# Kernel optimization log

Measured on AMD Instinct MI355X. Metric: run time of the kernel, lower is better.

The kernel has to match this reference:

```python
import jax, jax.numpy as jnp
import numpy as np

DIM = 128
NUM_LAYERS = 4
VOCAB = 32000
B, S = 32, 256


def setup_inputs() -> dict:
    key = jax.random.key(0)
    ks = jax.random.split(key, 8)
    sc = 1.0 / np.sqrt(DIM)
    return {
        "x": jax.random.randint(ks[0], (B, S), 0, VOCAB, dtype=jnp.int32),
        "emb": jax.random.normal(ks[1], (VOCAB, DIM), jnp.float32) * 0.02,
        "W_ih": jax.random.uniform(ks[2], (NUM_LAYERS, 4 * DIM, DIM), jnp.float32, -sc, sc),
        "W_hh": jax.random.uniform(ks[3], (NUM_LAYERS, 4 * DIM, DIM), jnp.float32, -sc, sc),
        "b_ih": jax.random.uniform(ks[4], (NUM_LAYERS, 4 * DIM), jnp.float32, -sc, sc),
        "b_hh": jax.random.uniform(ks[5], (NUM_LAYERS, 4 * DIM), jnp.float32, -sc, sc),
        "ln_gamma": jnp.ones((DIM,), jnp.float32),
        "ln_beta": jnp.zeros((DIM,), jnp.float32),
        "head_W": jax.random.uniform(ks[6], (VOCAB, DIM), jnp.float32, -sc, sc),
        "head_b": jnp.zeros((VOCAB,), jnp.float32),
    }


def _lstm_layer(h_seq, Wih, Whh, bih, bhh):
    # h_seq: [B,S,D]. Precompute input contributions for all timesteps.
    xW = jnp.einsum("bsd,gd->bsg", h_seq, Wih) + bih + bhh  # [B,S,4D]
    xW = jnp.swapaxes(xW, 0, 1)  # [S,B,4D] for scan over time
    bsz = h_seq.shape[0]
    h0 = jnp.zeros((bsz, DIM), h_seq.dtype)
    c0 = jnp.zeros((bsz, DIM), h_seq.dtype)

    def step(carry, xw_t):
        h, c = carry
        gates = xw_t + h @ Whh.T  # [B,4D]
        i, f, g, o = jnp.split(gates, 4, axis=-1)  # torch gate order i,f,g,o
        i = jax.nn.sigmoid(i)
        f = jax.nn.sigmoid(f)
        g = jnp.tanh(g)
        o = jax.nn.sigmoid(o)
        c = f * c + i * g
        h = o * jnp.tanh(c)
        return (h, c), h

    _, hs = jax.lax.scan(step, (h0, c0), xW)
    return jnp.swapaxes(hs, 0, 1)  # [B,S,D]


def reference(x, emb, W_ih, W_hh, b_ih, b_hh, ln_gamma, ln_beta, head_W, head_b):
    h = emb[x]  # [B,S,D]
    for l in range(NUM_LAYERS):
        h = _lstm_layer(h, W_ih[l], W_hh[l], b_ih[l], b_hh[l])
    # LayerNorm over last dim (eps=1e-5, torch default)
    mu = jnp.mean(h, axis=-1, keepdims=True)
    var = jnp.mean(jnp.square(h - mu), axis=-1, keepdims=True)
    hn = (h - mu) * jax.lax.rsqrt(var + 1e-5) * ln_gamma + ln_beta
    return jnp.einsum("bsd,vd->bsv", hn, head_W) + head_b  # [B,S,V]
```

## Files before the change

kernel.cpp:

```cpp
#include <hip/hip_runtime.h>
#include <hip/hip_bf16.h>

#define DIM 128
#define G4 512
#define NL 4
#define VOCAB 32000
#define BB 32
#define SS 256
#define ROWS (BB*SS)

typedef __attribute__((ext_vector_type(8))) short short8;
typedef __attribute__((ext_vector_type(4))) float f32x4;
typedef __attribute__((ext_vector_type(4))) unsigned int uint4v;
typedef __attribute__((ext_vector_type(2))) _Float16 h2;

__device__ __forceinline__ float fexp_(float x){ return __builtin_amdgcn_exp2f(x * 1.44269504088896f); }
__device__ __forceinline__ float frcp_(float x){ return __builtin_amdgcn_rcpf(x); }
__device__ __forceinline__ float sigm_(float x){ return frcp_(1.f + fexp_(-x)); }
__device__ __forceinline__ float tanh_(float x){
    float ax = fabsf(x);
    float e = fexp_(-2.f * ax);
    float t = (1.f - e) * frcp_(1.f + e);
    return x < 0.f ? -t : t;
}
__device__ __forceinline__ h2 mkh(float a, float b){ h2 r; r.x = (_Float16)a; r.y = (_Float16)b; return r; }

#if __has_builtin(__builtin_amdgcn_fdot2)
#define FDOT2(w, d, acc) acc = __builtin_amdgcn_fdot2(w, d, acc, false);
#else
#define FDOT2(w, d, acc) acc = fmaf((float)(w).x, (float)(d).x, fmaf((float)(w).y, (float)(d).y, acc));
#endif
#define B2H(u) __builtin_bit_cast(h2, (unsigned)(u))
#define F2US(x) ((unsigned long long)__builtin_bit_cast(unsigned short, (_Float16)(x)))

#define WD32(p) h2 p##0,p##1,p##2,p##3,p##4,p##5,p##6,p##7,p##8,p##9,p##10,p##11, \
                   p##12,p##13,p##14,p##15,p##16,p##17,p##18,p##19,p##20,p##21,p##22,p##23, \
                   p##24,p##25,p##26,p##27,p##28,p##29,p##30,p##31;
#define WCVT32(p, src) { float4 t_; \
    t_=(src)[0];  p##0 =mkh(t_.x,t_.y); p##1 =mkh(t_.z,t_.w); \
    t_=(src)[1];  p##2 =mkh(t_.x,t_.y); p##3 =mkh(t_.z,t_.w); \
    t_=(src)[2];  p##4 =mkh(t_.x,t_.y); p##5 =mkh(t_.z,t_.w); \
    t_=(src)[3];  p##6 =mkh(t_.x,t_.y); p##7 =mkh(t_.z,t_.w); \
    t_=(src)[4];  p##8 =mkh(t_.x,t_.y); p##9 =mkh(t_.z,t_.w); \
    t_=(src)[5];  p##10=mkh(t_.x,t_.y); p##11=mkh(t_.z,t_.w); \
    t_=(src)[6];  p##12=mkh(t_.x,t_.y); p##13=mkh(t_.z,t_.w); \
    t_=(src)[7];  p##14=mkh(t_.x,t_.y); p##15=mkh(t_.z,t_.w); \
    t_=(src)[8];  p##16=mkh(t_.x,t_.y); p##17=mkh(t_.z,t_.w); \
    t_=(src)[9];  p##18=mkh(t_.x,t_.y); p##19=mkh(t_.z,t_.w); \
    t_=(src)[10]; p##20=mkh(t_.x,t_.y); p##21=mkh(t_.z,t_.w); \
    t_=(src)[11]; p##22=mkh(t_.x,t_.y); p##23=mkh(t_.z,t_.w); \
    t_=(src)[12]; p##24=mkh(t_.x,t_.y); p##25=mkh(t_.z,t_.w); \
    t_=(src)[13]; p##26=mkh(t_.x,t_.y); p##27=mkh(t_.z,t_.w); \
    t_=(src)[14]; p##28=mkh(t_.x,t_.y); p##29=mkh(t_.z,t_.w); \
    t_=(src)[15]; p##30=mkh(t_.x,t_.y); p##31=mkh(t_.z,t_.w); }
#define DT32(p, acc) \
    FDOT2(p##0,d0,acc)  FDOT2(p##1,d1,acc)  FDOT2(p##2,d2,acc)  FDOT2(p##3,d3,acc) \
    FDOT2(p##4,d4,acc)  FDOT2(p##5,d5,acc)  FDOT2(p##6,d6,acc)  FDOT2(p##7,d7,acc) \
    FDOT2(p##8,d8,acc)  FDOT2(p##9,d9,acc)  FDOT2(p##10,d10,acc) FDOT2(p##11,d11,acc) \
    FDOT2(p##12,d12,acc) FDOT2(p##13,d13,acc) FDOT2(p##14,d14,acc) FDOT2(p##15,d15,acc) \
    FDOT2(p##16,d16,acc) FDOT2(p##17,d17,acc) FDOT2(p##18,d18,acc) FDOT2(p##19,d19,acc) \
    FDOT2(p##20,d20,acc) FDOT2(p##21,d21,acc) FDOT2(p##22,d22,acc) FDOT2(p##23,d23,acc) \
    FDOT2(p##24,d24,acc) FDOT2(p##25,d25,acc) FDOT2(p##26,d26,acc) FDOT2(p##27,d27,acc) \
    FDOT2(p##28,d28,acc) FDOT2(p##29,d29,acc) FDOT2(p##30,d30,acc) FDOT2(p##31,d31,acc)
#define RD32(base) { const uint4v* hc_ = (const uint4v*)(base); \
    uint4v q0_=hc_[0], q1_=hc_[1], q2_=hc_[2], q3_=hc_[3], \
           q4_=hc_[4], q5_=hc_[5], q6_=hc_[6], q7_=hc_[7]; \
    d0=B2H(q0_.x); d1=B2H(q0_.y); d2=B2H(q0_.z); d3=B2H(q0_.w); \
    d4=B2H(q1_.x); d5=B2H(q1_.y); d6=B2H(q1_.z); d7=B2H(q1_.w); \
    d8=B2H(q2_.x); d9=B2H(q2_.y); d10=B2H(q2_.z); d11=B2H(q2_.w); \
    d12=B2H(q3_.x); d13=B2H(q3_.y); d14=B2H(q3_.z); d15=B2H(q3_.w); \
    d16=B2H(q4_.x); d17=B2H(q4_.y); d18=B2H(q4_.z); d19=B2H(q4_.w); \
    d20=B2H(q5_.x); d21=B2H(q5_.y); d22=B2H(q5_.z); d23=B2H(q5_.w); \
    d24=B2H(q6_.x); d25=B2H(q6_.y); d26=B2H(q6_.z); d27=B2H(q6_.w); \
    d28=B2H(q7_.x); d29=B2H(q7_.y); d30=B2H(q7_.z); d31=B2H(q7_.w); }

#define W_DECL_ALL \
    float4 w0,w1,w2,w3,w4,w5,w6,w7,w8,w9,w10,w11,w12,w13,w14,w15, \
           w16,w17,w18,w19,w20,w21,w22,w23,w24,w25,w26,w27,w28,w29,w30,w31;
#define W_LOAD(i) w##i = wr[i];
#define W_LOAD_ALL \
    W_LOAD(0) W_LOAD(1) W_LOAD(2) W_LOAD(3) W_LOAD(4) W_LOAD(5) W_LOAD(6) W_LOAD(7) \
    W_LOAD(8) W_LOAD(9) W_LOAD(10) W_LOAD(11) W_LOAD(12) W_LOAD(13) W_LOAD(14) W_LOAD(15) \
    W_LOAD(16) W_LOAD(17) W_LOAD(18) W_LOAD(19) W_LOAD(20) W_LOAD(21) W_LOAD(22) W_LOAD(23) \
    W_LOAD(24) W_LOAD(25) W_LOAD(26) W_LOAD(27) W_LOAD(28) W_LOAD(29) W_LOAD(30) W_LOAD(31)
#define FMA1(i, acc) acc = fmaf(h4[i].x, w##i.x, fmaf(h4[i].y, w##i.y, \
                      fmaf(h4[i].z, w##i.z, fmaf(h4[i].w, w##i.w, acc))));
#define DOT128(a0,a1,a2,a3) \
    FMA1(0,a0) FMA1(1,a0) FMA1(2,a0) FMA1(3,a0) FMA1(4,a0) FMA1(5,a0) FMA1(6,a0) FMA1(7,a0) \
    FMA1(8,a1) FMA1(9,a1) FMA1(10,a1) FMA1(11,a1) FMA1(12,a1) FMA1(13,a1) FMA1(14,a1) FMA1(15,a1) \
    FMA1(16,a2) FMA1(17,a2) FMA1(18,a2) FMA1(19,a2) FMA1(20,a2) FMA1(21,a2) FMA1(22,a2) FMA1(23,a2) \
    FMA1(24,a3) FMA1(25,a3) FMA1(26,a3) FMA1(27,a3) FMA1(28,a3) FMA1(29,a3) FMA1(30,a3) FMA1(31,a3)

__global__ void k_zero(int* __restrict__ f){ if (threadIdx.x < 96) f[threadIdx.x] = 0; }

__global__ void k_embed(const int* __restrict__ x, const float* __restrict__ emb,
                        float* __restrict__ hseq){
    int i = blockIdx.x * blockDim.x + threadIdx.x;
    int row = i >> 5;
    int d4  = i & 31;
    int tok = x[row];
    ((float4*)hseq)[i] = ((const float4*)emb)[tok * 32 + d4];
}

__global__ __launch_bounds__(512, 2) void k_xw(const float* __restrict__ hseq,
                                               const float* Wih,
                                               const float* __restrict__ bih,
                                               const float* __restrict__ bhh,
                                               float* xw){
    __shared__ float hs[32 * DIM];
    int g = threadIdx.x;
    int r0 = blockIdx.x * 32;
    {
        const float4* src = (const float4*)(hseq + (size_t)r0 * DIM);
        float4* dst = (float4*)hs;
        for (int j = g; j < 32 * 32; j += 512) dst[j] = src[j];
    }
    int gg = ((g & 3) << 7) + (g >> 2);
    const float4* wr = (const float4*)(Wih + (size_t)gg * DIM);
    W_DECL_ALL
    W_LOAD_ALL
    float bias = bih[gg] + bhh[gg];
    __syncthreads();
    for (int r = 0; r < 32; ++r){
        const float4* h4 = (const float4*)(hs + r * DIM);
        float a0 = bias, a1 = 0.f, a2 = 0.f, a3 = 0.f;
        DOT128(a0, a1, a2, a3)
        xw[(size_t)(r0 + r) * G4 + g] = (a0 + a1) + (a2 + a3);
    }
}

#define SCAN_STEP(XC, CH, I) { \
        h2 d0,d1,d2,d3,d4,d5,d6,d7,d8,d9,d10,d11,d12,d13,d14,d15, \
           d16,d17,d18,d19,d20,d21,d22,d23,d24,d25,d26,d27,d28,d29,d30,d31; \
        float s0 = XC.x, s1 = XC.y; \
        RD32(&hb[p][0]) \
        DT32(pA, s0) DT32(pC, s1) \
        RD32(&hb[p][64]) \
        DT32(pB, s0) DT32(pD, s1) \
        float o0 = __shfl_xor(s0, 1), o1 = __shfl_xor(s1, 1); \
        float i_pre = w ? o0 : s0, f_pre = w ? o1 : s1; \
        float g_pre = w ? s0 : o0, o_pre = w ? s1 : o1; \
        float iv = sigm_(i_pre), fv = sigm_(f_pre); \
        float gv = tanh_(g_pre), ov = sigm_(o_pre); \
        cc = fv * cc + iv * gv; \
        float h = ov * tanh_(cc); \
        if (!w) hb[p ^ 1][ci] = (_Float16)h; \
        else    stg[(CH) & 1][I][ci] = h; \
        __syncthreads(); \
        p ^= 1; }

#define XN_DOT(I) { \
        h2 d0,d1,d2,d3,d4,d5,d6,d7,d8,d9,d10,d11,d12,d13,d14,d15, \
           d16,d17,d18,d19,d20,d21,d22,d23,d24,d25,d26,d27,d28,d29,d30,d31; \
        float nx = biasv.x, ny = biasv.y; \
        RD32(hpF + (I) * 128) \
        DT32(pE, nx) DT32(pG, ny) \
        RD32(hpF + (I) * 128 + 64) \
        DT32(pF, nx) DT32(pH, ny) \
        xn##I.x = nx; xn##I.y = ny; }

__global__ __launch_bounds__(256, 1) void k_fused(
    const float* __restrict__ xw0,
    const float* Wih, const float* Whh,
    const float* __restrict__ bih, const float* __restrict__ bhh,
    unsigned long long* hf16,
    float* hseq3,
    int* flags)
{
    __shared__ _Float16 hb[2][DIM];
    __shared__ float    stg[2][16][DIM];
    __shared__ __align__(16) unsigned long long hp[512];
    const int tid = threadIdx.x;
    const int l = blockIdx.x >> 5, b = blockIdx.x & 31;
    const int ci = tid >> 1, w = tid & 1;
    const _Float16* hpF = (const _Float16*)hp;

    WD32(pA) WD32(pB) WD32(pC) WD32(pD)
    {
        const float* Wl = Whh + (size_t)l * G4 * DIM;
        const float4* r0 = (const float4*)(Wl + (size_t)((2 * w    ) * DIM + ci) * DIM);
        const float4* r1 = (const float4*)(Wl + (size_t)((2 * w + 1) * DIM + ci) * DIM);
        WCVT32(pA, r0) WCVT32(pB, r0 + 16)
        WCVT32(pC, r1) WCVT32(pD, r1 + 16)
    }
    WD32(pE) WD32(pF) WD32(pG) WD32(pH)
    float2 biasv = {0.f, 0.f};
    if (l > 0){
        const float* Vl = Wih + (size_t)l * G4 * DIM;
        const float4* q0 = (const float4*)(Vl + (size_t)((2 * w    ) * DIM + ci) * DIM);
        const float4* q1 = (const float4*)(Vl + (size_t)((2 * w + 1) * DIM + ci) * DIM);
        WCVT32(pE, q0) WCVT32(pF, q0 + 16)
        WCVT32(pG, q1) WCVT32(pH, q1 + 16)
        biasv.x = bih[l * G4 + (2 * w    ) * DIM + ci] + bhh[l * G4 + (2 * w    ) * DIM + ci];
        biasv.y = bih[l * G4 + (2 * w + 1) * DIM + ci] + bhh[l * G4 + (2 * w + 1) * DIM + ci];
    }
    unsigned long long*       pub = hf16 + (size_t)(l * 32 + b) * 8192;
    const unsigned long long* src = hf16 + (size_t)((l - 1) * 32 + b) * 8192;
    int* myflag = flags + (l * 32 + b);
    const int* inflag = flags + ((l - 1) * 32 + b);
    const float2* xw2 = (const float2*)(xw0 + (size_t)b * SS * G4);
    float* hout = hseq3 + (size_t)b * SS * DIM;

    float cc = 0.f;
    if (tid < DIM) hb[0][tid] = (_Float16)0.f;
    __syncthreads();
    int p = 0;
    int seen = 0;
    float2 xq0,xq1,xq2,xq3,xq4,xq5,xq6,xq7,xq8,xq9,xq10,xq11,xq12,xq13,xq14,xq15;
    float2 xn0,xn1,xn2,xn3,xn4,xn5,xn6,xn7,xn8,xn9,xn10,xn11,xn12,xn13,xn14,xn15;

#define BLOCK_WAIT(TGT) { int t_ = (TGT); if (seen < t_){ \
        if (tid == 0){ while (__hip_atomic_load(inflag, __ATOMIC_ACQUIRE, \
            __HIP_MEMORY_SCOPE_AGENT) < t_) __builtin_amdgcn_s_sleep(4); } \
        __syncthreads(); seen = t_; } }
#define STAGE(C) { const unsigned long long* s_ = src + (size_t)(C) * 512; \
        hp[tid]       = __hip_atomic_load(s_ + tid,       __ATOMIC_RELAXED, __HIP_MEMORY_SCOPE_AGENT); \
        hp[tid + 256] = __hip_atomic_load(s_ + tid + 256, __ATOMIC_RELAXED, __HIP_MEMORY_SCOPE_AGENT); }
#define FLUSH_PUB(C) { \
    _Pragma("unroll") \
    for (int j = 0; j < 2; ++j){ \
        int idx = j * 256 + tid; \
        int r = idx >> 5, c4 = idx & 31; \
        float4 v = *(const float4*)&stg[(C) & 1][r][c4 * 4]; \
        unsigned long long bits = F2US(v.x) | (F2US(v.y) << 16) | (F2US(v.z) << 32) | (F2US(v.w) << 48); \
        __hip_atomic_store(pub + (size_t)((C) * 16 + r) * 32 + c4, bits, \
                           __ATOMIC_RELAXED, __HIP_MEMORY_SCOPE_AGENT); \
    } }
#define FLUSH_F32(C) { \
    _Pragma("unroll") \
    for (int j = 0; j < 2; ++j){ \
        int idx = j * 256 + tid; \
        int r = idx >> 5, c4 = idx & 31; \
        float4 v = *(const float4*)&stg[(C) & 1][r][c4 * 4]; \
        *(float4*)(hout + (size_t)((C) * 16 + r) * DIM + c4 * 4) = v; \
    } }
#define XQ_FROM_XN \
    xq0=xn0; xq1=xn1; xq2=xn2; xq3=xn3; xq4=xn4; xq5=xn5; xq6=xn6; xq7=xn7; \
    xq8=xn8; xq9=xn9; xq10=xn10; xq11=xn11; xq12=xn12; xq13=xn13; xq14=xn14; xq15=xn15;

    if (l > 0){
        BLOCK_WAIT(1)
        STAGE(0)
        __syncthreads();
        XN_DOT(0)  XN_DOT(1)  XN_DOT(2)  XN_DOT(3)  XN_DOT(4)  XN_DOT(5)  XN_DOT(6)  XN_DOT(7)
        XN_DOT(8)  XN_DOT(9)  XN_DOT(10) XN_DOT(11) XN_DOT(12) XN_DOT(13) XN_DOT(14) XN_DOT(15)
        XQ_FROM_XN
    }

#pragma unroll 1
    for (int c = 0; c < 16; ++c){
        if (c > 0){
            if (l < 3) FLUSH_PUB(c - 1)
            else       FLUSH_F32(c - 1)
        }
        if (l == 0){
            const int t0 = c * 16;
            xq0  = xw2[(t0 +  0) * 256 + tid]; xq1  = xw2[(t0 +  1) * 256 + tid];
            xq2  = xw2[(t0 +  2) * 256 + tid]; xq3  = xw2[(t0 +  3) * 256 + tid];
            xq4  = xw2[(t0 +  4) * 256 + tid]; xq5  = xw2[(t0 +  5) * 256 + tid];
            xq6  = xw2[(t0 +  6) * 256 + tid]; xq7  = xw2[(t0 +  7) * 256 + tid];
            xq8  = xw2[(t0 +  8) * 256 + tid]; xq9  = xw2[(t0 +  9) * 256 + tid];
            xq10 = xw2[(t0 + 10) * 256 + tid]; xq11 = xw2[(t0 + 11) * 256 + tid];
            xq12 = xw2[(t0 + 12) * 256 + tid]; xq13 = xw2[(t0 + 13) * 256 + tid];
            xq14 = xw2[(t0 + 14) * 256 + tid]; xq15 = xw2[(t0 + 15) * 256 + tid];
        } else if (c < 15){
            BLOCK_WAIT(c + 2)
            STAGE(c + 1)
        }
        __syncthreads();
        if (l < 3 && c > 0 && tid == 0)
            __hip_atomic_store(myflag, c, __ATOMIC_RELEASE, __HIP_MEMORY_SCOPE_AGENT);
        const bool doXN = (l > 0) && (c < 15);
        if (doXN) XN_DOT(0)   SCAN_STEP(xq0,  c, 0)
        if (doXN) XN_DOT(1)   SCAN_STEP(xq1,  c, 1)
        if (doXN) XN_DOT(2)   SCAN_STEP(xq2,  c, 2)
        if (doXN) XN_DOT(3)   SCAN_STEP(xq3,  c, 3)
        if (doXN) XN_DOT(4)   SCAN_STEP(xq4,  c, 4)
        if (doXN) XN_DOT(5)   SCAN_STEP(xq5,  c, 5)
        if (doXN) XN_DOT(6)   SCAN_STEP(xq6,  c, 6)
        if (doXN) XN_DOT(7)   SCAN_STEP(xq7,  c, 7)
        if (doXN) XN_DOT(8)   SCAN_STEP(xq8,  c, 8)
        if (doXN) XN_DOT(9)   SCAN_STEP(xq9,  c, 9)
        if (doXN) XN_DOT(10)  SCAN_STEP(xq10, c, 10)
        if (doXN) XN_DOT(11)  SCAN_STEP(xq11, c, 11)
        if (doXN) XN_DOT(12)  SCAN_STEP(xq12, c, 12)
        if (doXN) XN_DOT(13)  SCAN_STEP(xq13, c, 13)
        if (doXN) XN_DOT(14)  SCAN_STEP(xq14, c, 14)
        if (doXN) XN_DOT(15)  SCAN_STEP(xq15, c, 15)
        if (doXN){ XQ_FROM_XN }
    }
    if (l < 3){
        FLUSH_PUB(15)
        __syncthreads();
        if (tid == 0)
            __hip_atomic_store(myflag, 16, __ATOMIC_RELEASE, __HIP_MEMORY_SCOPE_AGENT);
    } else {
        FLUSH_F32(15)
    }
#undef BLOCK_WAIT
#undef STAGE
#undef FLUSH_PUB
#undef FLUSH_F32
#undef XQ_FROM_XN
}

__global__ void k_ln(const float* __restrict__ hseq, const float* __restrict__ gamma,
                     const float* __restrict__ beta, __hip_bfloat16* __restrict__ hn){
    int wid = threadIdx.x >> 6;
    int lane = threadIdx.x & 63;
    int row = blockIdx.x * 4 + wid;
    float2 hv = ((const float2*)(hseq + (size_t)row * DIM))[lane];
    float s = hv.x + hv.y;
    float sq = fmaf(hv.x, hv.x, hv.y * hv.y);
    for (int off = 32; off; off >>= 1){ s += __shfl_xor(s, off); sq += __shfl_xor(sq, off); }
    float mu = s * (1.f / 128.f);
    float var = sq * (1.f / 128.f) - mu * mu;
    float inv = rsqrtf(var + 1e-5f);
    float2 gv = ((const float2*)gamma)[lane];
    float2 bv = ((const float2*)beta)[lane];
    __hip_bfloat162 pr;
    pr.x = __float2bfloat16((hv.x - mu) * inv * gv.x + bv.x);
    pr.y = __float2bfloat16((hv.y - mu) * inv * gv.y + bv.y);
    ((__hip_bfloat162*)hn)[(size_t)row * 64 + lane] = pr;
}

__global__ void k_cvt(const float* __restrict__ w, __hip_bfloat16* __restrict__ wb){
    int i = blockIdx.x * blockDim.x + threadIdx.x;
    float4 v = ((const float4*)w)[i];
    __hip_bfloat162 p0, p1;
    p0.x = __float2bfloat16(v.x); p0.y = __float2bfloat16(v.y);
    p1.x = __float2bfloat16(v.z); p1.y = __float2bfloat16(v.w);
    ((__hip_bfloat162*)wb)[2 * i]     = p0;
    ((__hip_bfloat162*)wb)[2 * i + 1] = p1;
}

__global__ __launch_bounds__(256) void k_head(const __hip_bfloat16* __restrict__ hn,
                                              const __hip_bfloat16* __restrict__ wb,
                                              const float* __restrict__ head_b,
                                              float* __restrict__ out){
    int bn = blockIdx.x;
    int bm = blockIdx.y;
    int wid = threadIdx.x >> 6;
    int lane = threadIdx.x & 63;
    int wr = wid >> 1, wc = wid & 1;
    int row0 = bm * 128 + wr * 64;
    int col0 = bn * 128 + wc * 64;
    const short* A  = (const short*)hn;
    const short* Bp = (const short*)wb;
    f32x4 zero = {0.f, 0.f, 0.f, 0.f};
    f32x4 acc[4][4];
#pragma unroll
    for (int i = 0; i < 4; ++i)
#pragma unroll
        for (int j = 0; j < 4; ++j) acc[i][j] = zero;
    int lrow = lane & 15;
    int kgr = (lane >> 4) * 8;
#pragma unroll
    for (int ks = 0; ks < 4; ++ks){
        short8 a[4], bf[4];
#pragma unroll
        for (int mi = 0; mi < 4; ++mi)
            a[mi] = *(const short8*)(A + (size_t)(row0 + mi * 16 + lrow) * DIM + ks * 32 + kgr);
#pragma unroll
        for (int ni = 0; ni < 4; ++ni)
            bf[ni] = *(const short8*)(Bp + (size_t)(col0 + ni * 16 + lrow) * DIM + ks * 32 + kgr);
#pragma unroll
        for (int mi = 0; mi < 4; ++mi)
#pragma unroll
            for (int ni = 0; ni < 4; ++ni)
                acc[mi][ni] = __builtin_amdgcn_mfma_f32_16x16x32_bf16(bf[ni], a[mi], acc[mi][ni], 0, 0, 0);
    }
    int csub = (lane >> 4) * 4;
#pragma unroll
    for (int ni = 0; ni < 4; ++ni){
        int cbase = col0 + ni * 16 + csub;
        float4 b4 = ((const float4*)head_b)[cbase >> 2];
#pragma unroll
        for (int mi = 0; mi < 4; ++mi){
            int row = row0 + mi * 16 + lrow;
            f32x4 v;
            v[0] = acc[mi][ni][0] + b4.x;
            v[1] = acc[mi][ni][1] + b4.y;
            v[2] = acc[mi][ni][2] + b4.z;
            v[3] = acc[mi][ni][3] + b4.w;
            __builtin_nontemporal_store(v, (f32x4*)(out + (size_t)row * VOCAB + cbase));
        }
    }
}

extern "C" void kernel_launch(void* const* d_in, const int* in_sizes, int n_in,
                              void* d_out, int out_size, void* d_ws, size_t ws_size,
                              hipStream_t stream){
    const int*   x     = (const int*)  d_in[0];
    const float* emb   = (const float*)d_in[1];
    const float* Wih   = (const float*)d_in[2];
    const float* Whh   = (const float*)d_in[3];
    const float* bih   = (const float*)d_in[4];
    const float* bhh   = (const float*)d_in[5];
    const float* gamma = (const float*)d_in[6];
    const float* beta  = (const float*)d_in[7];
    const float* headW = (const float*)d_in[8];
    const float* headb = (const float*)d_in[9];
    float* out = (float*)d_out;

    char* ws = (char*)d_ws;
    float* xw0  = (float*)ws;
    float* hseq = (float*)(ws + (16u << 20));
    __hip_bfloat16* hn = (__hip_bfloat16*)(ws + (20u << 20));
    __hip_bfloat16* wb = (__hip_bfloat16*)(ws + (22u << 20));

    char* ob = (char*)d_out;
    unsigned long long* hf16 = (unsigned long long*)ob;
    int* flags = (int*)(ob + (6u << 20));

    k_embed<<<1024, 256, 0, stream>>>(x, emb, hseq);
    k_cvt  <<<4000, 256, 0, stream>>>(headW, wb);
    k_xw   <<<256, 512, 0, stream>>>(hseq, Wih, bih, bhh, xw0);
    k_zero <<<1, 128, 0, stream>>>(flags);
    k_fused<<<128, 256, 0, stream>>>(xw0, Wih, Whh, bih, bhh, hf16, hseq, flags);
    k_ln   <<<2048, 256, 0, stream>>>(hseq, gamma, beta, hn);
    k_head <<<dim3(250, 64), 256, 0, stream>>>(hn, wb, headb, out);
}
```

Before: 782.8 us.

## Fuse embedding into xw, LayerNorm into LSTM kernel, halve chunk size

Folds the embedding gather into the input-projection kernel and stores the layer-0 gate pre-activations as fp16 instead of fp32. LayerNorm moves into the last layer's flush inside the fused LSTM kernel, so the separate embed and LN kernels and the fp32 hidden-sequence round trip go away. Pipeline chunks shrink from 16 to 8 timesteps, which shortens the wait between layers in the wavefront at the cost of more flag syncs. It also pads LDS with a large unused array, presumably to limit co-residency, and adds a min-blocks hint on the head GEMM. The fp16 pre-activations cost some precision.

```diff
diff --git a/kernel.cpp b/kernel.cpp
--- a/kernel.cpp
+++ b/kernel.cpp
@@ -24,6 +24,15 @@
     return x < 0.f ? -t : t;
 }
 __device__ __forceinline__ h2 mkh(float a, float b){ h2 r; r.x = (_Float16)a; r.y = (_Float16)b; return r; }
+__device__ __forceinline__ unsigned long long f2bf_(float f){
+    unsigned u = __float_as_uint(f);
+    u += 0x7fffu + ((u >> 16) & 1u);
+    return (unsigned long long)(u >> 16);
+}
+__device__ __forceinline__ float2 c2f(unsigned u){
+    h2 v = __builtin_bit_cast(h2, u);
+    float2 r; r.x = (float)v.x; r.y = (float)v.y; return r;
+}
 
 #if __has_builtin(__builtin_amdgcn_fdot2)
 #define FDOT2(w, d, acc) acc = __builtin_amdgcn_fdot2(w, d, acc, false);
@@ -93,27 +102,22 @@
 
 __global__ void k_zero(int* __restrict__ f){ if (threadIdx.x < 96) f[threadIdx.x] = 0; }
 
-__global__ void k_embed(const int* __restrict__ x, const float* __restrict__ emb,
-                        float* __restrict__ hseq){
-    int i = blockIdx.x * blockDim.x + threadIdx.x;
-    int row = i >> 5;
-    int d4  = i & 31;
-    int tok = x[row];
-    ((float4*)hseq)[i] = ((const float4*)emb)[tok * 32 + d4];
-}
-
-__global__ __launch_bounds__(512, 2) void k_xw(const float* __restrict__ hseq,
+__global__ __launch_bounds__(512, 2) void k_xw(const int* __restrict__ x,
+                                               const float* __restrict__ emb,
                                                const float* Wih,
                                                const float* __restrict__ bih,
                                                const float* __restrict__ bhh,
-                                               float* xw){
+                                               unsigned short* xwh){
     __shared__ float hs[32 * DIM];
     int g = threadIdx.x;
     int r0 = blockIdx.x * 32;
     {
-        const float4* src = (const float4*)(hseq + (size_t)r0 * DIM);
         float4* dst = (float4*)hs;
-        for (int j = g; j < 32 * 32; j += 512) dst[j] = src[j];
+        for (int j = g; j < 32 * 32; j += 512){
+            int row = j >> 5, c4 = j & 31;
+            int tok = x[r0 + row];
+            dst[row * 32 + c4] = ((const float4*)emb)[tok * 32 + c4];
+        }
     }
     int gg = ((g & 3) << 7) + (g >> 2);
     const float4* wr = (const float4*)(Wih + (size_t)gg * DIM);
@@ -125,7 +129,8 @@
         const float4* h4 = (const float4*)(hs + r * DIM);
         float a0 = bias, a1 = 0.f, a2 = 0.f, a3 = 0.f;
         DOT128(a0, a1, a2, a3)
-        xw[(size_t)(r0 + r) * G4 + g] = (a0 + a1) + (a2 + a3);
+        float v = (a0 + a1) + (a2 + a3);
+        xwh[(size_t)(r0 + r) * G4 + g] = __builtin_bit_cast(unsigned short, (_Float16)v);
     }
 }
 
@@ -160,17 +165,22 @@
         xn##I.x = nx; xn##I.y = ny; }
 
 __global__ __launch_bounds__(256, 1) void k_fused(
-    const float* __restrict__ xw0,
+    const unsigned short* __restrict__ xw0h,
     const float* Wih, const float* Whh,
     const float* __restrict__ bih, const float* __restrict__ bhh,
     unsigned long long* hf16,
-    float* hseq3,
-    int* flags)
+    int* flags,
+    const float* __restrict__ gamma, const float* __restrict__ beta,
+    __hip_bfloat16* hnb,
+    int dummy)
 {
     __shared__ _Float16 hb[2][DIM];
-    __shared__ float    stg[2][16][DIM];
-    __shared__ __align__(16) unsigned long long hp[512];
+    __shared__ float    stg[2][8][DIM];
+    __shared__ __align__(16) unsigned long long hp[256];
+    __shared__ f32x4    lds_pad[5376];
     const int tid = threadIdx.x;
+    if (dummy) ((volatile float*)lds_pad)[tid] = 0.f;
+
     const int l = blockIdx.x >> 5, b = blockIdx.x & 31;
     const int ci = tid >> 1, w = tid & 1;
     const _Float16* hpF = (const _Float16*)hp;
@@ -198,130 +208,106 @@
     const unsigned long long* src = hf16 + (size_t)((l - 1) * 32 + b) * 8192;
     int* myflag = flags + (l * 32 + b);
     const int* inflag = flags + ((l - 1) * 32 + b);
-    const float2* xw2 = (const float2*)(xw0 + (size_t)b * SS * G4);
-    float* hout = hseq3 + (size_t)b * SS * DIM;
+    const unsigned* xwu = (const unsigned*)xw0h + (size_t)b * SS * 256;
+    unsigned long long* hn8 = (unsigned long long*)hnb;
 
     float cc = 0.f;
     if (tid < DIM) hb[0][tid] = (_Float16)0.f;
     __syncthreads();
     int p = 0;
     int seen = 0;
-    float2 xq0,xq1,xq2,xq3,xq4,xq5,xq6,xq7,xq8,xq9,xq10,xq11,xq12,xq13,xq14,xq15;
-    float2 xn0,xn1,xn2,xn3,xn4,xn5,xn6,xn7,xn8,xn9,xn10,xn11,xn12,xn13,xn14,xn15;
+    float2 xq0,xq1,xq2,xq3,xq4,xq5,xq6,xq7;
+    float2 xn0,xn1,xn2,xn3,xn4,xn5,xn6,xn7;
 
 #define BLOCK_WAIT(TGT) { int t_ = (TGT); if (seen < t_){ \
         if (tid == 0){ while (__hip_atomic_load(inflag, __ATOMIC_ACQUIRE, \
             __HIP_MEMORY_SCOPE_AGENT) < t_) __builtin_amdgcn_s_sleep(4); } \
         __syncthreads(); seen = t_; } }
-#define STAGE(C) { const unsigned long long* s_ = src + (size_t)(C) * 512; \
-        hp[tid]       = __hip_atomic_load(s_ + tid,       __ATOMIC_RELAXED, __HIP_MEMORY_SCOPE_AGENT); \
-        hp[tid + 256] = __hip_atomic_load(s_ + tid + 256, __ATOMIC_RELAXED, __HIP_MEMORY_SCOPE_AGENT); }
+#define STAGE(C) { const unsigned long long* s_ = src + (size_t)(C) * 256; \
+        hp[tid] = __hip_atomic_load(s_ + tid, __ATOMIC_RELAXED, __HIP_MEMORY_SCOPE_AGENT); }
 #define FLUSH_PUB(C) { \
-    _Pragma("unroll") \
-    for (int j = 0; j < 2; ++j){ \
-        int idx = j * 256 + tid; \
-        int r = idx >> 5, c4 = idx & 31; \
+        int r = tid >> 5, c4 = tid & 31; \
         float4 v = *(const float4*)&stg[(C) & 1][r][c4 * 4]; \
         unsigned long long bits = F2US(v.x) | (F2US(v.y) << 16) | (F2US(v.z) << 32) | (F2US(v.w) << 48); \
-        __hip_atomic_store(pub + (size_t)((C) * 16 + r) * 32 + c4, bits, \
-                           __ATOMIC_RELAXED, __HIP_MEMORY_SCOPE_AGENT); \
-    } }
-#define FLUSH_F32(C) { \
-    _Pragma("unroll") \
-    for (int j = 0; j < 2; ++j){ \
-        int idx = j * 256 + tid; \
-        int r = idx >> 5, c4 = idx & 31; \
+        __hip_atomic_store(pub + (size_t)((C) * 8 + r) * 32 + c4, bits, \
+                           __ATOMIC_RELAXED, __HIP_MEMORY_SCOPE_AGENT); }
+#define FLUSH_LN(C) { \
+        int r = tid >> 5, c4 = tid & 31; \
         float4 v = *(const float4*)&stg[(C) & 1][r][c4 * 4]; \
-        *(float4*)(hout + (size_t)((C) * 16 + r) * DIM + c4 * 4) = v; \
-    } }
-#define XQ_FROM_XN \
-    xq0=xn0; xq1=xn1; xq2=xn2; xq3=xn3; xq4=xn4; xq5=xn5; xq6=xn6; xq7=xn7; \
-    xq8=xn8; xq9=xn9; xq10=xn10; xq11=xn11; xq12=xn12; xq13=xn13; xq14=xn14; xq15=xn15;
+        float s_ = (v.x + v.y) + (v.z + v.w); \
+        float q_ = fmaf(v.x, v.x, fmaf(v.y, v.y, fmaf(v.z, v.z, v.w * v.w))); \
+        s_ += __shfl_xor(s_, 1);  q_ += __shfl_xor(q_, 1); \
+        s_ += __shfl_xor(s_, 2);  q_ += __shfl_xor(q_, 2); \
+        s_ += __shfl_xor(s_, 4);  q_ += __shfl_xor(q_, 4); \
+        s_ += __shfl_xor(s_, 8);  q_ += __shfl_xor(q_, 8); \
+        s_ += __shfl_xor(s_, 16); q_ += __shfl_xor(q_, 16); \
+        float mu_ = s_ * (1.f / 128.f); \
+        float var_ = q_ * (1.f / 128.f) - mu_ * mu_; \
+        float inv_ = rsqrtf(var_ + 1e-5f); \
+        float4 gv_ = ((const float4*)gamma)[c4]; \
+        float4 bv_ = ((const float4*)beta)[c4]; \
+        unsigned long long bits = \
+              f2bf_((v.x - mu_) * inv_ * gv_.x + bv_.x) \
+            | (f2bf_((v.y - mu_) * inv_ * gv_.y + bv_.y) << 16) \
+            | (f2bf_((v.z - mu_) * inv_ * gv_.z + bv_.z) << 32) \
+            | (f2bf_((v.w - mu_) * inv_ * gv_.w + bv_.w) << 48); \
+        int grow = b * 256 + (C) * 8 + r; \
+        *(unsigned long long*)(hn8 + (size_t)grow * 32 + c4) = bits; }
+#define XQ_FROM_XN xq0=xn0; xq1=xn1; xq2=xn2; xq3=xn3; xq4=xn4; xq5=xn5; xq6=xn6; xq7=xn7;
 
     if (l > 0){
         BLOCK_WAIT(1)
         STAGE(0)
         __syncthreads();
-        XN_DOT(0)  XN_DOT(1)  XN_DOT(2)  XN_DOT(3)  XN_DOT(4)  XN_DOT(5)  XN_DOT(6)  XN_DOT(7)
-        XN_DOT(8)  XN_DOT(9)  XN_DOT(10) XN_DOT(11) XN_DOT(12) XN_DOT(13) XN_DOT(14) XN_DOT(15)
+        XN_DOT(0) XN_DOT(1) XN_DOT(2) XN_DOT(3) XN_DOT(4) XN_DOT(5) XN_DOT(6) XN_DOT(7)
         XQ_FROM_XN
     }
 
 #pragma unroll 1
-    for (int c = 0; c < 16; ++c){
+    for (int c = 0; c < 32; ++c){
         if (c > 0){
             if (l < 3) FLUSH_PUB(c - 1)
-            else       FLUSH_F32(c - 1)
+            else       FLUSH_LN(c - 1)
         }
         if (l == 0){
-            const int t0 = c * 16;
-            xq0  = xw2[(t0 +  0) * 256 + tid]; xq1  = xw2[(t0 +  1) * 256 + tid];
-            xq2  = xw2[(t0 +  2) * 256 + tid]; xq3  = xw2[(t0 +  3) * 256 + tid];
-            xq4  = xw2[(t0 +  4) * 256 + tid]; xq5  = xw2[(t0 +  5) * 256 + tid];
-            xq6  = xw2[(t0 +  6) * 256 + tid]; xq7  = xw2[(t0 +  7) * 256 + tid];
-            xq8  = xw2[(t0 +  8) * 256 + tid]; xq9  = xw2[(t0 +  9) * 256 + tid];
-            xq10 = xw2[(t0 + 10) * 256 + tid]; xq11 = xw2[(t0 + 11) * 256 + tid];
-            xq12 = xw2[(t0 + 12) * 256 + tid]; xq13 = xw2[(t0 + 13) * 256 + tid];
-            xq14 = xw2[(t0 + 14) * 256 + tid]; xq15 = xw2[(t0 + 15) * 256 + tid];
-        } else if (c < 15){
+            const int t0 = c * 8;
+            unsigned u0 = xwu[(t0 + 0) * 256 + tid], u1 = xwu[(t0 + 1) * 256 + tid],
+                     u2 = xwu[(t0 + 2) * 256 + tid], u3 = xwu[(t0 + 3) * 256 + tid],
+                     u4 = xwu[(t0 + 4) * 256 + tid], u5 = xwu[(t0 + 5) * 256 + tid],
+                     u6 = xwu[(t0 + 6) * 256 + tid], u7 = xwu[(t0 + 7) * 256 + tid];
+            xq0 = c2f(u0); xq1 = c2f(u1); xq2 = c2f(u2); xq3 = c2f(u3);
+            xq4 = c2f(u4); xq5 = c2f(u5); xq6 = c2f(u6); xq7 = c2f(u7);
+        } else if (c < 31){
             BLOCK_WAIT(c + 2)
             STAGE(c + 1)
         }
         __syncthreads();
         if (l < 3 && c > 0 && tid == 0)
             __hip_atomic_store(myflag, c, __ATOMIC_RELEASE, __HIP_MEMORY_SCOPE_AGENT);
-        const bool doXN = (l > 0) && (c < 15);
-        if (doXN) XN_DOT(0)   SCAN_STEP(xq0,  c, 0)
-        if (doXN) XN_DOT(1)   SCAN_STEP(xq1,  c, 1)
-        if (doXN) XN_DOT(2)   SCAN_STEP(xq2,  c, 2)
-        if (doXN) XN_DOT(3)   SCAN_STEP(xq3,  c, 3)
-        if (doXN) XN_DOT(4)   SCAN_STEP(xq4,  c, 4)
-        if (doXN) XN_DOT(5)   SCAN_STEP(xq5,  c, 5)
-        if (doXN) XN_DOT(6)   SCAN_STEP(xq6,  c, 6)
-        if (doXN) XN_DOT(7)   SCAN_STEP(xq7,  c, 7)
-        if (doXN) XN_DOT(8)   SCAN_STEP(xq8,  c, 8)
-        if (doXN) XN_DOT(9)   SCAN_STEP(xq9,  c, 9)
-        if (doXN) XN_DOT(10)  SCAN_STEP(xq10, c, 10)
-        if (doXN) XN_DOT(11)  SCAN_STEP(xq11, c, 11)
-        if (doXN) XN_DOT(12)  SCAN_STEP(xq12, c, 12)
-        if (doXN) XN_DOT(13)  SCAN_STEP(xq13, c, 13)
-        if (doXN) XN_DOT(14)  SCAN_STEP(xq14, c, 14)
-        if (doXN) XN_DOT(15)  SCAN_STEP(xq15, c, 15)
+        const bool doXN = (l > 0) && (c < 31);
+        if (doXN) XN_DOT(0)  SCAN_STEP(xq0, c, 0)
+        if (doXN) XN_DOT(1)  SCAN_STEP(xq1, c, 1)
+        if (doXN) XN_DOT(2)  SCAN_STEP(xq2, c, 2)
+        if (doXN) XN_DOT(3)  SCAN_STEP(xq3, c, 3)
+        if (doXN) XN_DOT(4)  SCAN_STEP(xq4, c, 4)
+        if (doXN) XN_DOT(5)  SCAN_STEP(xq5, c, 5)
+        if (doXN) XN_DOT(6)  SCAN_STEP(xq6, c, 6)
+        if (doXN) XN_DOT(7)  SCAN_STEP(xq7, c, 7)
         if (doXN){ XQ_FROM_XN }
     }
     if (l < 3){
-        FLUSH_PUB(15)
+        FLUSH_PUB(31)
         __syncthreads();
         if (tid == 0)
-            __hip_atomic_store(myflag, 16, __ATOMIC_RELEASE, __HIP_MEMORY_SCOPE_AGENT);
+            __hip_atomic_store(myflag, 32, __ATOMIC_RELEASE, __HIP_MEMORY_SCOPE_AGENT);
     } else {
-        FLUSH_F32(15)
+        FLUSH_LN(31)
     }
 #undef BLOCK_WAIT
 #undef STAGE
 #undef FLUSH_PUB
-#undef FLUSH_F32
+#undef FLUSH_LN
 #undef XQ_FROM_XN
-}
-
-__global__ void k_ln(const float* __restrict__ hseq, const float* __restrict__ gamma,
-                     const float* __restrict__ beta, __hip_bfloat16* __restrict__ hn){
-    int wid = threadIdx.x >> 6;
-    int lane = threadIdx.x & 63;
-    int row = blockIdx.x * 4 + wid;
-    float2 hv = ((const float2*)(hseq + (size_t)row * DIM))[lane];
-    float s = hv.x + hv.y;
-    float sq = fmaf(hv.x, hv.x, hv.y * hv.y);
-    for (int off = 32; off; off >>= 1){ s += __shfl_xor(s, off); sq += __shfl_xor(sq, off); }
-    float mu = s * (1.f / 128.f);
-    float var = sq * (1.f / 128.f) - mu * mu;
-    float inv = rsqrtf(var + 1e-5f);
-    float2 gv = ((const float2*)gamma)[lane];
-    float2 bv = ((const float2*)beta)[lane];
-    __hip_bfloat162 pr;
-    pr.x = __float2bfloat16((hv.x - mu) * inv * gv.x + bv.x);
-    pr.y = __float2bfloat16((hv.y - mu) * inv * gv.y + bv.y);
-    ((__hip_bfloat162*)hn)[(size_t)row * 64 + lane] = pr;
 }
 
 __global__ void k_cvt(const float* __restrict__ w, __hip_bfloat16* __restrict__ wb){
@@ -334,10 +320,10 @@
     ((__hip_bfloat162*)wb)[2 * i + 1] = p1;
 }
 
-__global__ __launch_bounds__(256) void k_head(const __hip_bfloat16* __restrict__ hn,
-                                              const __hip_bfloat16* __restrict__ wb,
-                                              const float* __restrict__ head_b,
-                                              float* __restrict__ out){
+__global__ __launch_bounds__(256, 3) void k_head(const __hip_bfloat16* __restrict__ hn,
+                                                 const __hip_bfloat16* __restrict__ wb,
+                                                 const float* __restrict__ head_b,
+                                                 float* __restrict__ out){
     int bn = blockIdx.x;
     int bm = blockIdx.y;
     int wid = threadIdx.x >> 6;
@@ -404,20 +390,16 @@
     float* out = (float*)d_out;
 
     char* ws = (char*)d_ws;
-    float* xw0  = (float*)ws;
-    float* hseq = (float*)(ws + (16u << 20));
-    __hip_bfloat16* hn = (__hip_bfloat16*)(ws + (20u << 20));
-    __hip_bfloat16* wb = (__hip_bfloat16*)(ws + (22u << 20));
-
-    char* ob = (char*)d_out;
-    unsigned long long* hf16 = (unsigned long long*)ob;
-    int* flags = (int*)(ob + (6u << 20));
-
-    k_embed<<<1024, 256, 0, stream>>>(x, emb, hseq);
+    unsigned short* xw0h = (unsigned short*)ws;
+    unsigned long long* hf16 = (unsigned long long*)(ws + (8u << 20));
+    __hip_bfloat16* hn = (__hip_bfloat16*)(ws + (14u << 20));
+    __hip_bfloat16* wb = (__hip_bfloat16*)(ws + (16u << 20));
+    int* flags = (int*)(ws + (24u << 20));
+
     k_cvt  <<<4000, 256, 0, stream>>>(headW, wb);
-    k_xw   <<<256, 512, 0, stream>>>(hseq, Wih, bih, bhh, xw0);
+    k_xw   <<<256, 512, 0, stream>>>(x, emb, Wih, bih, bhh, xw0h);
     k_zero <<<1, 128, 0, stream>>>(flags);
-    k_fused<<<128, 256, 0, stream>>>(xw0, Wih, Whh, bih, bhh, hf16, hseq, flags);
-    k_ln   <<<2048, 256, 0, stream>>>(hseq, gamma, beta, hn);
+    k_fused<<<128, 256, 0, stream>>>(xw0h, Wih, Whh, bih, bhh, hf16, flags,
+                                     gamma, beta, hn, 0);
     k_head <<<dim3(250, 64), 256, 0, stream>>>(hn, wb, headb, out);
 }
```

Result: no change. 795.3 us (+1.6%).
